# Performance work log

Measured on AMD Instinct MI355X. Metric: run time of the kernel, lower is better.

## Reference

```python
import jax, jax.numpy as jnp
import numpy as np

MARGIN = 0.5

def setup_inputs() -> dict:
    key = jax.random.key(0)
    k1, k2 = jax.random.split(key)
    n, d, n_classes = 8192, 512, 1024
    embedding = jax.random.normal(k1, (n, d), dtype=jnp.float32)
    label = jax.random.randint(k2, (n,), 0, n_classes, dtype=jnp.int64)
    return {"embedding": embedding, "label": label}


def reference(embedding, label):
    # sim_mat[i, j] = <e_i, e_j>
    n = embedding.shape[0]
    sim = embedding @ embedding.T  # [n, n]
    same = label[:, None] == label[None, :]  # [n, n] bool
    # per-row positive pairs: same label AND sim < 1; loss contrib (1 - sim)
    pos_mask = same & (sim < 1.0)
    # per-row negative pairs (hard mining): diff label AND sim > margin; loss contrib sim
    neg_mask = (~same) & (sim > MARGIN)
    pos_loss = jnp.sum(jnp.where(pos_mask, 1.0 - sim, 0.0))
    neg_loss = jnp.sum(jnp.where(neg_mask, sim, 0.0))
    loss = (pos_loss + neg_loss) / n
    return (loss, 0, 0)
```

## Files before the change

kernel.cpp:

```cpp
#include <hip/hip_runtime.h>
#include <hip/hip_bf16.h>


typedef int   i32x4 __attribute__((ext_vector_type(4)));

#define N_EMB 8192
#define D_EMB 512
#define BM    128
#define HKB   64
#define NPH   (D_EMB / HKB)
#define TILES (N_EMB / BM)
#define NBLK  (TILES * (TILES + 1) / 2)
#define MARGIN_F 0.5f
#define QSCALE 24.0f
#define DEQ    (1.0f / (QSCALE * QSCALE))
#define HBYT  (BM * HKB)

__device__ __forceinline__ void gll16(const void* g, void* l) {
    __builtin_amdgcn_global_load_lds(
        (const __attribute__((address_space(1))) void*)g,
        (__attribute__((address_space(3))) void*)l,
        16 , 0 , 0 );
}

__global__ __launch_bounds__(256) void quant_kernel(const float* __restrict__ in,
                                                    int4* __restrict__ out, int n16) {
    int i = blockIdx.x * blockDim.x + threadIdx.x;
    if (i >= n16) return;
    const float4* p = reinterpret_cast<const float4*>(in) + i * 4;
    int4 o;
    int* po = reinterpret_cast<int*>(&o);
#pragma unroll
    for (int j = 0; j < 4; ++j) {
        float4 v = p[j];
        int b0 = (int)rintf(fminf(fmaxf(v.x * QSCALE, -127.f), 127.f));
        int b1 = (int)rintf(fminf(fmaxf(v.y * QSCALE, -127.f), 127.f));
        int b2 = (int)rintf(fminf(fmaxf(v.z * QSCALE, -127.f), 127.f));
        int b3 = (int)rintf(fminf(fmaxf(v.w * QSCALE, -127.f), 127.f));
        po[j] = (b0 & 255) | ((b1 & 255) << 8) | ((b2 & 255) << 16) | ((b3 & 255) << 24);
    }
    out[i] = o;
}

__global__ __launch_bounds__(256) void loss_kernel(const char* __restrict__ E8,
                                                   const int* __restrict__ label,
                                                   float* __restrict__ partials) {
    const int bid = blockIdx.x;
    const int t = (bid & 7) * (NBLK / 8) + (bid >> 3);

    int tr = (int)(64.5f - sqrtf(4160.25f - 2.0f * (float)t));
    while ((tr + 1) * TILES - ((tr + 1) * tr) / 2 <= t) ++tr;
    while (tr * TILES - (tr * (tr - 1)) / 2 > t) --tr;
    const int tc = tr + (t - (tr * TILES - (tr * (tr - 1)) / 2));

    __shared__ char  lds[3][2][HBYT];
    __shared__ float red[4];

    const int tid  = threadIdx.x;
    const int wid  = tid >> 6, lane = tid & 63;
    const int wrow = wid >> 1, wcol = wid & 1;
    const int fr   = lane & 15;
    const int kq   = lane >> 4;
    const int row0 = tr * BM, col0 = tc * BM;

    const int sw = (((tid & 3) ^ ((tid >> 2) & 3)) << 4);
    const int r0 = tid >> 2, r1 = 64 + (tid >> 2);
    const char* gA0 = E8 + (size_t)(row0 + r0) * D_EMB + sw;
    const char* gA1 = E8 + (size_t)(row0 + r1) * D_EMB + sw;
    const char* gB0 = E8 + (size_t)(col0 + r0) * D_EMB + sw;
    const char* gB1 = E8 + (size_t)(col0 + r1) * D_EMB + sw;
    const int d0 = tid << 4;
    const int d1 = (tid + 256) << 4;

    i32x4 acc[4][4] = {};

    const int psw = ((kq ^ (fr & 3)) << 4);

    gll16(gA0,       &lds[0][0][d0]); gll16(gA1,       &lds[0][0][d1]);
    gll16(gB0,       &lds[0][1][d0]); gll16(gB1,       &lds[0][1][d1]);
    gll16(gA0 + HKB, &lds[1][0][d0]); gll16(gA1 + HKB, &lds[1][0][d1]);
    gll16(gB0 + HKB, &lds[1][1][d0]); gll16(gB1 + HKB, &lds[1][1][d1]);

#pragma unroll
    for (int p = 0; p < NPH; ++p) {
        const int rg = p % 3;
        if (p < NPH - 1) {
            asm volatile("s_waitcnt vmcnt(4)" ::: "memory");
        } else {
            asm volatile("s_waitcnt vmcnt(0)" ::: "memory");
        }
        __builtin_amdgcn_s_barrier();

        if (p + 2 < NPH) {
            const int rg2 = (p + 2) % 3;
            const int ko  = (p + 2) * HKB;
            gll16(gA0 + ko, &lds[rg2][0][d0]); gll16(gA1 + ko, &lds[rg2][0][d1]);
            gll16(gB0 + ko, &lds[rg2][1][d0]); gll16(gB1 + ko, &lds[rg2][1][d1]);
        }

        i32x4 a[4], b[4];
#pragma unroll
        for (int m = 0; m < 4; ++m)
            a[m] = *reinterpret_cast<const i32x4*>(
                &lds[rg][0][((wrow * 64 + m * 16 + fr) << 6) + psw]);
#pragma unroll
        for (int n = 0; n < 4; ++n)
            b[n] = *reinterpret_cast<const i32x4*>(
                &lds[rg][1][((wcol * 64 + n * 16 + fr) << 6) + psw]);
        asm volatile("s_waitcnt lgkmcnt(0)" ::: "memory");
        __builtin_amdgcn_sched_barrier(0);
        __builtin_amdgcn_s_setprio(1);
#pragma unroll
        for (int m = 0; m < 4; ++m)
#pragma unroll
            for (int n = 0; n < 4; ++n)
                acc[m][n] = __builtin_amdgcn_mfma_i32_16x16x64_i8(a[m], b[n], acc[m][n], 0, 0, 0);
        __builtin_amdgcn_s_setprio(0);
    }

    float local = 0.f;
    int lj[4];
#pragma unroll
    for (int n = 0; n < 4; ++n) lj[n] = label[col0 + wcol * 64 + n * 16 + fr];
    const int rb = kq << 2;
#pragma unroll
    for (int m = 0; m < 4; ++m) {
#pragma unroll
        for (int r = 0; r < 4; ++r) {
            const int li = label[row0 + wrow * 64 + m * 16 + rb + r];
#pragma unroll
            for (int n = 0; n < 4; ++n) {
                const float s = (float)acc[m][n][r] * DEQ;
                if (li == lj[n]) {
                    if (s < 1.0f) local += 1.0f - s;
                } else if (s > MARGIN_F) {
                    local += s;
                }
            }
        }
    }
    if (tr != tc) local *= 2.0f;

#pragma unroll
    for (int off = 32; off > 0; off >>= 1) local += __shfl_xor(local, off);
    if (lane == 0) red[wid] = local;
    __syncthreads();
    if (tid == 0) partials[t] = red[0] + red[1] + red[2] + red[3];
}

__global__ __launch_bounds__(256) void reduce_kernel(const float* __restrict__ partials,
                                                     float* __restrict__ out, int nb) {
    float s = 0.f;
    for (int i = threadIdx.x; i < nb; i += 256) s += partials[i];
#pragma unroll
    for (int off = 32; off > 0; off >>= 1) s += __shfl_xor(s, off);
    __shared__ float red[4];
    if ((threadIdx.x & 63) == 0) red[threadIdx.x >> 6] = s;
    __syncthreads();
    if (threadIdx.x == 0) {
        out[0] = (red[0] + red[1] + red[2] + red[3]) * (1.0f / (float)N_EMB);
        out[1] = 0.f;
        out[2] = 0.f;
    }
}

extern "C" void kernel_launch(void* const* d_in, const int* in_sizes, int n_in,
                              void* d_out, int out_size, void* d_ws, size_t ws_size,
                              hipStream_t stream) {
    const float* emb   = (const float*)d_in[0];
    const int*   label = (const int*)d_in[1];
    float*       out   = (float*)d_out;

    char*  E8      = (char*)d_ws;
    float* partial = (float*)((char*)d_ws + (size_t)N_EMB * D_EMB);

    const int n16 = N_EMB * D_EMB / 16;
    quant_kernel<<<(n16 + 255) / 256, 256, 0, stream>>>(emb, (int4*)E8, n16);

    loss_kernel<<<NBLK, 256, 0, stream>>>(E8, label, partial);

    reduce_kernel<<<1, 256, 0, stream>>>(partial, out, NBLK);
}
```

Baseline: 46.39 us.

## Make loss kernel persistent with cross-tile prefetch pipeline

Replaces the launch of one block per triangular tile with a 512-block persistent grid in which each block walks 4 or 5 tiles. The 3-stage LDS load pipeline now runs continuously across tile boundaries: the next tile's addresses are computed mid-tile, so its first K-chunks are prefetched while the current tile finishes. The epilogue runs inline, after which the accumulators are cleared. This removes block launch and prologue/epilogue pipeline bubbles, but adds a non-unrolled loop with runtime branches and the load imbalance between blocks that do 4 tiles and blocks that do 5.

```diff
diff --git a/kernel.cpp b/kernel.cpp
--- a/kernel.cpp
+++ b/kernel.cpp
@@ -2,15 +2,17 @@
 #include <hip/hip_bf16.h>
 
 
-typedef int   i32x4 __attribute__((ext_vector_type(4)));
+typedef int i32x4 __attribute__((ext_vector_type(4)));
 
 #define N_EMB 8192
 #define D_EMB 512
 #define BM    128
 #define HKB   64
-#define NPH   (D_EMB / HKB)
-#define TILES (N_EMB / BM)
-#define NBLK  (TILES * (TILES + 1) / 2)
+#define NPH   8
+#define TILES 64
+#define NBLK  2080
+#define PERX  (NBLK / 8)
+#define GRID  512
 #define MARGIN_F 0.5f
 #define QSCALE 24.0f
 #define DEQ    (1.0f / (QSCALE * QSCALE))
@@ -21,6 +23,14 @@
         (const __attribute__((address_space(1))) void*)g,
         (__attribute__((address_space(3))) void*)l,
         16 , 0 , 0 );
+}
+
+__device__ __forceinline__ void decode_tile(int t, int& tr, int& tc) {
+    int r = (int)(64.5f - sqrtf(4160.25f - 2.0f * (float)t));
+    while ((r + 1) * TILES - ((r + 1) * r) / 2 <= t) ++r;
+    while (r * TILES - (r * (r - 1)) / 2 > t) --r;
+    tr = r;
+    tc = r + (t - (r * TILES - (r * (r - 1)) / 2));
 }
 
 __global__ __launch_bounds__(256) void quant_kernel(const float* __restrict__ in,
@@ -45,13 +55,10 @@
 __global__ __launch_bounds__(256) void loss_kernel(const char* __restrict__ E8,
                                                    const int* __restrict__ label,
                                                    float* __restrict__ partials) {
-    const int bid = blockIdx.x;
-    const int t = (bid & 7) * (NBLK / 8) + (bid >> 3);
-
-    int tr = (int)(64.5f - sqrtf(4160.25f - 2.0f * (float)t));
-    while ((tr + 1) * TILES - ((tr + 1) * tr) / 2 <= t) ++tr;
-    while (tr * TILES - (tr * (tr - 1)) / 2 > t) --tr;
-    const int tc = tr + (t - (tr * TILES - (tr * (tr - 1)) / 2));
+    const int bid  = blockIdx.x;
+    const int xcd  = bid & 7, slot = bid >> 3;
+    const int ntile = (slot < (PERX - 4 * 64)) ? 5 : 4;
+    const int W = ntile * NPH;
 
     __shared__ char  lds[3][2][HBYT];
     __shared__ float red[4];
@@ -61,39 +68,45 @@
     const int wrow = wid >> 1, wcol = wid & 1;
     const int fr   = lane & 15;
     const int kq   = lane >> 4;
-    const int row0 = tr * BM, col0 = tc * BM;
 
     const int sw = (((tid & 3) ^ ((tid >> 2) & 3)) << 4);
     const int r0 = tid >> 2, r1 = 64 + (tid >> 2);
-    const char* gA0 = E8 + (size_t)(row0 + r0) * D_EMB + sw;
-    const char* gA1 = E8 + (size_t)(row0 + r1) * D_EMB + sw;
-    const char* gB0 = E8 + (size_t)(col0 + r0) * D_EMB + sw;
-    const char* gB1 = E8 + (size_t)(col0 + r1) * D_EMB + sw;
-    const int d0 = tid << 4;
-    const int d1 = (tid + 256) << 4;
+    const int d0 = tid << 4, d1 = (tid + 256) << 4;
+    const int psw = ((kq ^ (fr & 3)) << 4);
+
+    int rd_t = xcd * PERX + slot;
+    int tr, tc;
+    decode_tile(rd_t, tr, tc);
+    int rd_row0 = tr * BM, rd_col0 = tc * BM;
+    int nx_row0 = rd_row0, nx_col0 = rd_col0;
+
+    const char* gA0 = E8 + (size_t)(rd_row0 + r0) * D_EMB + sw;
+    const char* gA1 = E8 + (size_t)(rd_row0 + r1) * D_EMB + sw;
+    const char* gB0 = E8 + (size_t)(rd_col0 + r0) * D_EMB + sw;
+    const char* gB1 = E8 + (size_t)(rd_col0 + r1) * D_EMB + sw;
 
     i32x4 acc[4][4] = {};
-
-    const int psw = ((kq ^ (fr & 3)) << 4);
+    float lane_sum = 0.f;
 
     gll16(gA0,       &lds[0][0][d0]); gll16(gA1,       &lds[0][0][d1]);
     gll16(gB0,       &lds[0][1][d0]); gll16(gB1,       &lds[0][1][d1]);
     gll16(gA0 + HKB, &lds[1][0][d0]); gll16(gA1 + HKB, &lds[1][0][d1]);
     gll16(gB0 + HKB, &lds[1][1][d0]); gll16(gB1 + HKB, &lds[1][1][d1]);
 
-#pragma unroll
-    for (int p = 0; p < NPH; ++p) {
-        const int rg = p % 3;
-        if (p < NPH - 1) {
+    int ktile = 0;
+#pragma unroll 1
+    for (int w = 0; w < W; ++w) {
+        const int rg = w % 3;
+        if (w < W - 1) {
             asm volatile("s_waitcnt vmcnt(4)" ::: "memory");
         } else {
             asm volatile("s_waitcnt vmcnt(0)" ::: "memory");
         }
         __builtin_amdgcn_s_barrier();
 
-        if (p + 2 < NPH) {
-            const int rg2 = (p + 2) % 3;
-            const int ko  = (p + 2) * HKB;
+        if (w + 2 < W) {
+            const int rg2 = (w + 2) % 3;
+            const int ko  = ((w + 2) & 7) * HKB;
             gll16(gA0 + ko, &lds[rg2][0][d0]); gll16(gA1 + ko, &lds[rg2][0][d1]);
             gll16(gB0 + ko, &lds[rg2][1][d0]); gll16(gB1 + ko, &lds[rg2][1][d1]);
         }
@@ -116,36 +129,57 @@
             for (int n = 0; n < 4; ++n)
                 acc[m][n] = __builtin_amdgcn_mfma_i32_16x16x64_i8(a[m], b[n], acc[m][n], 0, 0, 0);
         __builtin_amdgcn_s_setprio(0);
-    }
-
-    float local = 0.f;
-    int lj[4];
-#pragma unroll
-    for (int n = 0; n < 4; ++n) lj[n] = label[col0 + wcol * 64 + n * 16 + fr];
-    const int rb = kq << 2;
-#pragma unroll
-    for (int m = 0; m < 4; ++m) {
-#pragma unroll
-        for (int r = 0; r < 4; ++r) {
-            const int li = label[row0 + wrow * 64 + m * 16 + rb + r];
-#pragma unroll
-            for (int n = 0; n < 4; ++n) {
-                const float s = (float)acc[m][n][r] * DEQ;
-                if (li == lj[n]) {
-                    if (s < 1.0f) local += 1.0f - s;
-                } else if (s > MARGIN_F) {
-                    local += s;
+
+        const int ph = w & 7;
+        if (ph == 5 && ktile + 1 < ntile) {
+            int tn = rd_t + 64;
+            int tr2, tc2;
+            decode_tile(tn, tr2, tc2);
+            nx_row0 = tr2 * BM; nx_col0 = tc2 * BM;
+            gA0 = E8 + (size_t)(nx_row0 + r0) * D_EMB + sw;
+            gA1 = E8 + (size_t)(nx_row0 + r1) * D_EMB + sw;
+            gB0 = E8 + (size_t)(nx_col0 + r0) * D_EMB + sw;
+            gB1 = E8 + (size_t)(nx_col0 + r1) * D_EMB + sw;
+        }
+        if (ph == 7) {
+            float local = 0.f;
+            int lj[4];
+#pragma unroll
+            for (int n = 0; n < 4; ++n)
+                lj[n] = label[rd_col0 + wcol * 64 + n * 16 + fr];
+            const int rb = kq << 2;
+#pragma unroll
+            for (int m = 0; m < 4; ++m) {
+#pragma unroll
+                for (int r = 0; r < 4; ++r) {
+                    const int li = label[rd_row0 + wrow * 64 + m * 16 + rb + r];
+#pragma unroll
+                    for (int n = 0; n < 4; ++n) {
+                        const float s = (float)acc[m][n][r] * DEQ;
+                        if (li == lj[n]) {
+                            if (s < 1.0f) local += 1.0f - s;
+                        } else if (s > MARGIN_F) {
+                            local += s;
+                        }
+                    }
                 }
             }
+            lane_sum += (rd_row0 != rd_col0) ? 2.0f * local : local;
+#pragma unroll
+            for (int m = 0; m < 4; ++m)
+#pragma unroll
+                for (int n = 0; n < 4; ++n)
+                    acc[m][n] = i32x4{0, 0, 0, 0};
+            rd_t += 64; rd_row0 = nx_row0; rd_col0 = nx_col0;
+            ++ktile;
         }
     }
-    if (tr != tc) local *= 2.0f;
-
-#pragma unroll
-    for (int off = 32; off > 0; off >>= 1) local += __shfl_xor(local, off);
-    if (lane == 0) red[wid] = local;
+
+#pragma unroll
+    for (int off = 32; off > 0; off >>= 1) lane_sum += __shfl_xor(lane_sum, off);
+    if (lane == 0) red[wid] = lane_sum;
     __syncthreads();
-    if (tid == 0) partials[t] = red[0] + red[1] + red[2] + red[3];
+    if (tid == 0) partials[bid] = red[0] + red[1] + red[2] + red[3];
 }
 
 __global__ __launch_bounds__(256) void reduce_kernel(const float* __restrict__ partials,
@@ -177,7 +211,7 @@
     const int n16 = N_EMB * D_EMB / 16;
     quant_kernel<<<(n16 + 255) / 256, 256, 0, stream>>>(emb, (int4*)E8, n16);
 
-    loss_kernel<<<NBLK, 256, 0, stream>>>(E8, label, partial);
-
-    reduce_kernel<<<1, 256, 0, stream>>>(partial, out, NBLK);
-}
+    loss_kernel<<<GRID, 256, 0, stream>>>(E8, label, partial);
+
+    reduce_kernel<<<1, 256, 0, stream>>>(partial, out, GRID);
+}
```

Result: slower. 70.68 us (+52.3%).
